# Kernel tuning notes

Measured on AMD Instinct MI355X. Metric: run time of the kernel, lower is better.

The kernel has to match this reference:

```python
import jax, jax.numpy as jnp
import numpy as np
from jax import lax

BG_THRESHOLD = -0.5
KEEP_COMPONENTS = 2
MIN_AREA = 200.0
N_ITERS = 32  # fixed label-propagation sweeps; each sweep does full-row/col run propagation + 3x3 max-pool (8-connectivity), plenty for blobby CT masks


def _conv_ones(x, k):
    kern = jnp.ones((1, 1, k, k), x.dtype)
    return lax.conv_general_dilated(x, kern, (1, 1), 'SAME',
                                    dimension_numbers=('NCHW', 'OIHW', 'NCHW'))


def _morph_open(m):
    # erode: all 9 neighbors set; dilate: any neighbor set (matches torch conv2d thresholds)
    e = (_conv_ones(m, 3) == 9.0).astype(m.dtype)
    return (_conv_ones(e, 3) > 0.0).astype(m.dtype)


def _fill_holes(m):
    # binary closing with 5x5 kernel
    d = (_conv_ones(m, 5) > 0.0).astype(m.dtype)
    return (_conv_ones(d, 5) == 25.0).astype(m.dtype)


def _prop_last(lab, msk):
    # propagate running max of labels along last axis, resetting at mask==0 (run propagation)
    lW = jnp.moveaxis(lab, -1, 0)  # [W,B,H]
    mW = jnp.moveaxis(msk, -1, 0)
    def step(c, lm):
        l, m = lm
        c = jnp.where(m, jnp.maximum(c, l), 0)
        return c, c
    _, out = lax.scan(step, jnp.zeros(lW.shape[1:], lab.dtype), (lW, mW))
    return jnp.moveaxis(out, 0, -1)


def _ccl_labels(msk):
    # 8-connected component labeling via iterative max-label propagation.
    # msk: bool [B,H,W]. Returns int32 labels (0 = background); pixels in the
    # same component converge to the same (max) seed label.
    B, H, W = msk.shape
    seeds = (jnp.arange(H * W, dtype=jnp.int32) + 1).reshape(H, W)
    lab0 = jnp.where(msk, seeds[None], 0)
    mi = msk.astype(jnp.int32)

    def body(i, lab):
        # diagonal hop (8-connectivity)
        lab = lax.reduce_window(lab, jnp.int32(0), lax.max,
                                (1, 3, 3), (1, 1, 1), 'SAME') * mi
        # full-run propagation left->right, right->left
        lab = _prop_last(lab, msk)
        lab = jnp.flip(_prop_last(jnp.flip(lab, -1), jnp.flip(msk, -1)), -1)
        # top->bottom, bottom->top
        labT = jnp.swapaxes(lab, -1, -2)
        mskT = jnp.swapaxes(msk, -1, -2)
        labT = _prop_last(labT, mskT)
        labT = jnp.flip(_prop_last(jnp.flip(labT, -1), jnp.flip(mskT, -1)), -1)
        return jnp.swapaxes(labT, -1, -2)

    return lax.fori_loop(0, N_ITERS, body, lab0)


def _keep_largest_components(mask4):
    # mask4: [B,1,H,W] float in {0,1}
    B, _, H, W = mask4.shape
    msk = mask4[:, 0] > 0.5
    labels = _ccl_labels(lax.stop_gradient(msk))  # int32 [B,H,W]
    # per-batch area histogram over label ids (label values in [0, H*W])
    def areas_fn(l, m):
        return jnp.zeros(H * W + 1, jnp.float32).at[l.ravel()].add(
            m.ravel().astype(jnp.float32))
    areas = jax.vmap(areas_fn)(labels, msk)          # [B, H*W+1]
    areas = areas.at[:, 0].set(0.0)                  # background excluded
    areas = jnp.where(areas >= MIN_AREA, areas, 0.0) # drop small noise regions
    topv, topi = lax.top_k(areas, KEEP_COMPONENTS)   # [B,K]
    topi = jnp.where(topv > 0.0, topi, -1)           # invalidate empty slots
    keep = jnp.any(labels[..., None] == topi[:, None, None, :], axis=-1)
    return keep.astype(mask4.dtype)[:, None]         # [B,1,H,W]


def setup_inputs() -> dict:
    key = jax.random.key(0)
    x = jax.random.normal(key, (64, 1, 512, 512), dtype=jnp.float32)
    return {"x": x}


def reference(x):
    m = (x > BG_THRESHOLD).astype(x.dtype)
    m = _morph_open(m)
    m = _keep_largest_components(m)
    m = _fill_holes(m)
    return m
```

## Files before the change

kernel.cpp:

```cpp
#include <hip/hip_runtime.h>
#include <stdint.h>
#include <limits.h>

#define BB 64
#define HH 512
#define WW 512
#define WPR 8
#define WPRP 9
#define HWP (HH*WW)
#define NPIX (BB*HWP)
#define NROWS (BB*HH)
#define RS 128
#define RSP 129
#define MAXRUNS (NROWS*RS)
#define KPR 32
#define MAXROOTS 2048

typedef unsigned char u8;
typedef unsigned long long u64;

__device__ __forceinline__ int imax(int a, int b){ return a > b ? a : b; }

__device__ __forceinline__ u64 hshift3_and(u64 c, u64 l, u64 r){
  return c & ((c << 1) | (l >> 63)) & ((c >> 1) | (r << 63));
}
__device__ __forceinline__ u64 hshift3_or(u64 c, u64 l, u64 r){
  return c | (c << 1) | (l >> 63) | (c >> 1) | (r << 63);
}
__device__ __forceinline__ u64 hshift5_and(u64 c, u64 l, u64 r){
  return hshift3_and(c, l, r) & ((c << 2) | (l >> 62)) & ((c >> 2) | (r << 62));
}
__device__ __forceinline__ u64 hshift5_or(u64 c, u64 l, u64 r){
  return hshift3_or(c, l, r) | (c << 2) | (l >> 62) | (c >> 2) | (r << 62);
}

__device__ __forceinline__ int lfind(int* lp, int p){
  while (true){
    int q = lp[p];
    int g = lp[q];
    if (q == g) return q;
    atomicMin(&lp[p], g);
    p = g;
  }
}
__device__ __forceinline__ void lunion(int* lp, int a, int b){
  while (true){
    a = lfind(lp, a);
    b = lfind(lp, b);
    if (a == b) return;
    if (a < b){ int t = a; a = b; b = t; }
    int old = atomicMin(&lp[a], b);
    if (old == a) return;
    a = old;
  }
}

#define ORPB 16
#define TPR (256/ORPB)
#define SLABN (ORPB*RS)
__global__ __launch_bounds__(256)
void k_thropen(const float* __restrict__ x, uint32_t* __restrict__ runs,
               int* __restrict__ cnt, int* __restrict__ parent,
               int* __restrict__ area, int* __restrict__ clabel,
               int* __restrict__ rootcnt){
  __shared__ u64 thr[ORPB + 4][WPRP];
  __shared__ u64 er[ORPB + 2][WPRP];
  __shared__ u64 dl[ORPB][WPRP];
  __shared__ uint32_t lruns[ORPB][RSP];
  __shared__ int lcnt[ORPB];
  __shared__ int lparent[SLABN];
  int R0 = blockIdx.x * ORPB;
  int img = R0 >> 9;
  int y0 = R0 & (HH - 1);
  int wid  = threadIdx.x >> 6;
  int lane = threadIdx.x & 63;
  if (blockIdx.x == 0 && threadIdx.x < BB) rootcnt[threadIdx.x] = 0;

  for (int pair = wid; pair < (ORPB + 4)/2; pair += 4){
    int lrow = 2*pair + (lane >> 5);
    int y = y0 - 2 + lrow;
    unsigned m = 0;
    if ((unsigned)y < (unsigned)HH){
      const float4* X = reinterpret_cast<const float4*>(
          x + ((size_t)img*HH + y)*WW + (lane & 31)*16);
      #pragma unroll
      for (int q = 0; q < 4; ++q){
        float4 vv = X[q];
        m |= (unsigned)(vv.x > -0.5f) << (q*4 + 0);
        m |= (unsigned)(vv.y > -0.5f) << (q*4 + 1);
        m |= (unsigned)(vv.z > -0.5f) << (q*4 + 2);
        m |= (unsigned)(vv.w > -0.5f) << (q*4 + 3);
      }
    }
    int sub = lane & 3;
    unsigned p1 = __shfl_xor(m, 1);
    unsigned v32 = (sub & 1) ? (p1 | (m << 16)) : (m | (p1 << 16));
    unsigned p2 = __shfl_xor(v32, 2);
    if (sub == 0)
      thr[lrow][(lane >> 2) & 7] = (u64)v32 | ((u64)p2 << 32);
  }
  __syncthreads();

  for (int s = threadIdx.x; s < (ORPB + 2)*WPR; s += 256){
    int j = s >> 3;
    int wi = s & 7;
    int rr = y0 - 1 + j;
    u64 acc = ~0ULL;
    #pragma unroll
    for (int dy = 0; dy < 3; ++dy){
      int ti = j + dy;
      u64 c = thr[ti][wi];
      u64 l = (wi > 0) ? thr[ti][wi-1] : 0ULL;
      u64 r = (wi < 7) ? thr[ti][wi+1] : 0ULL;
      acc &= hshift3_and(c, l, r);
    }
    if ((unsigned)rr >= (unsigned)HH) acc = 0ULL;
    er[j][wi] = acc;
  }
  __syncthreads();

  for (int s = threadIdx.x; s < ORPB*WPR; s += 256){
    int ri = s >> 3;
    int wi = s & 7;
    u64 acc = 0ULL;
    #pragma unroll
    for (int dy = 0; dy < 3; ++dy){
      int li = ri + dy;
      u64 c = er[li][wi];
      u64 l = (wi > 0) ? er[li][wi-1] : 0ULL;
      u64 r = (wi < 7) ? er[li][wi+1] : 0ULL;
      acc |= hshift3_or(c, l, r);
    }
    dl[ri][wi] = acc;
  }
  __syncthreads();

  for (int i = threadIdx.x; i < SLABN; i += 256) lparent[i] = i;

  if (threadIdx.x < ORPB){
    int ri = threadIdx.x;
    int r = R0 + ri;
    u64 w[8];
    #pragma unroll
    for (int i = 0; i < 8; ++i) w[i] = dl[ri][i];
    int base = r*RS;
    int k = 0;
    int pending = -1;
    u64 carry = 0;
    #pragma unroll
    for (int wi = 0; wi < 8; ++wi){
      u64 b = w[wi];
      u64 nb0 = (wi < 7) ? (w[wi+1] & 1ULL) : 0ULL;
      u64 starts = b & ~((b << 1) | carry);
      u64 ends   = b & ~(b >> 1);
      if (nb0) ends &= ~(1ULL << 63);
      carry = b >> 63;
      while (ends){
        int e = __ffsll((long long)ends) - 1; ends &= ends - 1;
        int s;
        if (pending >= 0){ s = pending; pending = -1; }
        else { s = wi*64 + (__ffsll((long long)starts) - 1); starts &= starts - 1; }
        uint32_t rv = (uint32_t)s | ((uint32_t)(wi*64 + e) << 16);
        int id = base + k;
        runs[id] = rv; lruns[ri][k] = rv;
        area[id] = 0; clabel[id] = 0;
        k++;
      }
      if (starts) pending = wi*64 + (__ffsll((long long)starts) - 1);
    }
    cnt[r] = k; lcnt[ri] = k;
  }
  __syncthreads();

  {
    int ri = threadIdx.x / TPR;
    int k0 = threadIdx.x % TPR;
    if (ri > 0){
      int ca = lcnt[ri], cb = lcnt[ri-1];
      if (cb > 0){
        for (int k = k0; k < ca; k += TPR){
          uint32_t ra = lruns[ri][k]; int sA = (int)(ra & 0xffff), eA = (int)(ra >> 16);
          int lo = 0, hi = cb, target = sA - 1;
          while (lo < hi){
            int mid = (lo + hi) >> 1;
            if ((int)(lruns[ri-1][mid] >> 16) < target) lo = mid + 1; else hi = mid;
          }
          for (int j = lo; j < cb; ++j){
            if ((int)(lruns[ri-1][j] & 0xffff) > eA + 1) break;
            lunion(lparent, ri*RS + k, (ri-1)*RS + j);
          }
        }
      }
    }
  }
  __syncthreads();

  {
    int ri = threadIdx.x / TPR;
    int k0 = threadIdx.x % TPR;
    int n = lcnt[ri];
    for (int k = k0; k < n; k += TPR){
      int lid = ri*RS + k;
      parent[R0*RS + lid] = R0*RS + lfind(lparent, lid);
    }
  }
}

__device__ __forceinline__ int uf_find(int* parent, int p){
  while (true){
    int q = parent[p];
    int g = parent[q];
    if (q == g) return q;
    atomicMin(&parent[p], g);
    p = g;
  }
}
__device__ __forceinline__ void uf_union(int* parent, int a, int b){
  while (true){
    a = uf_find(parent, a);
    b = uf_find(parent, b);
    if (a == b) return;
    if (a < b){ int t = a; a = b; b = t; }
    int old = atomicMin(&parent[a], b);
    if (old == a) return;
    a = old;
  }
}

__device__ __forceinline__ int ro_find(const int* __restrict__ parent, int p){
  while (true){ int q = parent[p]; if (q == p) return p; p = q; }
}

#define NBND (HH/ORPB - 1)
__global__ void k_linkb(const uint32_t* __restrict__ runs, const int* __restrict__ cnt,
                        int* __restrict__ parent){
  int t = blockIdx.x*blockDim.x + threadIdx.x;
  int bi = t >> 3, k0 = t & 7;
  if (bi >= BB*NBND) return;
  int img = bi / NBND, j = bi % NBND;
  int r = img*HH + (j + 1)*ORPB;
  int ca = cnt[r];
  int cb = cnt[r-1];
  if (cb == 0) return;
  const uint32_t* RB = runs + (size_t)(r-1)*RS;
  for (int k = k0; k < ca; k += 8){
    int id = r*RS + k;
    uint32_t ra = runs[id]; int sA = (int)(ra & 0xffff), eA = (int)(ra >> 16);
    int lo = 0, hi = cb, target = sA - 1;
    while (lo < hi){
      int mid = (lo + hi) >> 1;
      if ((int)(RB[mid] >> 16) < target) lo = mid + 1; else hi = mid;
    }
    for (int jj = lo; jj < cb; ++jj){
      uint32_t rb = RB[jj];
      if ((int)(rb & 0xffff) > eA + 1) break;
      uf_union(parent, id, (r-1)*RS + jj);
    }
  }
}

__global__ __launch_bounds__(256)
void k_slabacc(const uint32_t* __restrict__ runs, const int* __restrict__ cnt,
               int* __restrict__ parent, int* __restrict__ area,
               int* __restrict__ clabel){
  __shared__ int larea[SLABN];
  __shared__ int lclab[SLABN];
  for (int i = threadIdx.x; i < SLABN; i += 256){ larea[i] = 0; lclab[i] = 0; }
  __syncthreads();
  int R0 = blockIdx.x * ORPB;
  int base = R0 * RS;
  int y0 = R0 & (HH - 1);
  int ri = threadIdx.x / TPR;
  int k0 = threadIdx.x % TPR;
  int r = R0 + ri;
  int n = cnt[r];
  for (int k = k0; k < n; k += TPR){
    int id = r*RS + k;
    uint32_t run = runs[id]; int s = (int)(run & 0xffff), e = (int)(run >> 16);
    int len = e - s + 1;
    int labl = ri*WW + e + 1;
    int p = parent[id];
    int lid = p - base;
    if ((unsigned)lid < (unsigned)SLABN){
      atomicAdd(&larea[lid], len);
      atomicMax(&lclab[lid], labl);
    } else {
      p = ro_find(parent, p);
      atomicAdd(&area[p], len);
      atomicMax(&clabel[p], y0*WW + labl);
    }
  }
  __syncthreads();
  for (int i = threadIdx.x; i < SLABN; i += 256){
    int la = larea[i];
    if (la == 0) continue;
    int gid = base + i;
    int p = ro_find(parent, gid);
    atomicAdd(&area[p], la);
    atomicMax(&clabel[p], y0*WW + lclab[i]);
    if (p != gid) parent[gid] = p;
  }
}

__global__ void k_roots(const int* __restrict__ cnt, const int* __restrict__ parent,
                        const int* __restrict__ area, const int* __restrict__ clabel,
                        int* __restrict__ rootcnt, int* __restrict__ rootA,
                        int* __restrict__ rootL){
  int t = blockIdx.x*blockDim.x + threadIdx.x;
  if (t >= NROWS*KPR) return;
  int r = t / KPR, k0 = t % KPR;
  int n = cnt[r];
  int b = r >> 9;
  for (int k = k0; k < n; k += KPR){
    int id = r*RS + k;
    if (parent[id] != id) continue;
    int a = area[id];
    if (a < 200) continue;
    int idx = atomicAdd(&rootcnt[b], 1);
    rootA[b*MAXROOTS + idx] = a;
    rootL[b*MAXROOTS + idx] = clabel[id];
  }
}

__device__ __forceinline__ void ins2(int v, int i, int& v1, int& i1, int& v2, int& i2){
  if (v > v1 || (v == v1 && i < i1)) { v2 = v1; i2 = i1; v1 = v; i1 = i; }
  else if (v > v2 || (v == v2 && i < i2)) { v2 = v; i2 = i; }
}

__global__ void k_top2(const int* __restrict__ rootcnt, const int* __restrict__ rootA,
                       const int* __restrict__ rootL, int* __restrict__ keepL){
  __shared__ int sv1[64], si1[64], sv2[64], si2[64];
  int b = blockIdx.x;
  int n = rootcnt[b];
  int v1 = 0, i1 = INT_MAX, v2 = 0, i2 = INT_MAX;
  for (int k = threadIdx.x; k < n; k += 64)
    ins2(rootA[b*MAXROOTS + k], rootL[b*MAXROOTS + k], v1, i1, v2, i2);
  int t = threadIdx.x;
  sv1[t] = v1; si1[t] = i1; sv2[t] = v2; si2[t] = i2;
  __syncthreads();
  for (int s = 32; s > 0; s >>= 1){
    if (t < s){
      int a1 = sv1[t], b1 = si1[t], a2 = sv2[t], b2 = si2[t];
      ins2(sv1[t+s], si1[t+s], a1, b1, a2, b2);
      ins2(sv2[t+s], si2[t+s], a1, b1, a2, b2);
      sv1[t] = a1; si1[t] = b1; sv2[t] = a2; si2[t] = b2;
    }
    __syncthreads();
  }
  if (t == 0){
    keepL[b*2 + 0] = (sv1[0] > 0) ? si1[0] : 0;
    keepL[b*2 + 1] = (sv2[0] > 0) ? si2[0] : 0;
  }
}

__device__ __forceinline__ u64 rmask(int s, int e){
  u64 hi = (e >= 63) ? ~0ULL : ((1ULL << (e + 1)) - 1);
  u64 lo = (1ULL << s) - 1;
  return hi & ~lo;
}

#define CRPB 32
__global__ __launch_bounds__(256)
void k_closeexpand(const uint32_t* __restrict__ runs, const int* __restrict__ cnt,
                   const int* __restrict__ parent, const int* __restrict__ clabel,
                   const int* __restrict__ keepL, float* __restrict__ out){
  __shared__ u64 kp[CRPB + 8][WPR];
  __shared__ u64 dil[CRPB + 4][WPR];
  __shared__ u64 ero[CRPB][WPR];
  __shared__ int scnt[CRPB + 8];
  int R0 = blockIdx.x * CRPB;
  int img = R0 >> 9;
  int y0 = R0 & (HH - 1);
  int L1 = keepL[img*2], L2 = keepL[img*2 + 1];
  for (int i = threadIdx.x; i < (CRPB + 8)*WPR; i += 256)
    kp[i >> 3][i & 7] = 0ULL;
  if (threadIdx.x < CRPB + 8){
    int y = y0 + threadIdx.x - 4;
    scnt[threadIdx.x] = ((unsigned)y < (unsigned)HH) ? cnt[img*HH + y] : 0;
  }
  __syncthreads();
  for (int rr = threadIdx.x >> 3; rr < CRPB + 8; rr += 32){
    int y = y0 + rr - 4;
    int row = img*HH + y;
    int n = scnt[rr];
    for (int k = threadIdx.x & 7; k < n; k += 8){
      int id = row*RS + k;
      int p = parent[id];
      while (true){ int q = parent[p]; if (q == p) break; p = q; }
      int L = clabel[p];
      if (L != L1 && L != L2) continue;
      uint32_t run = runs[id]; int st = (int)(run & 0xffff), e = (int)(run >> 16);
      int w0 = st >> 6, w1 = e >> 6;
      if (w0 == w1) atomicOr(&kp[rr][w0], rmask(st & 63, e & 63));
      else {
        atomicOr(&kp[rr][w0], rmask(st & 63, 63));
        for (int wi = w0 + 1; wi < w1; ++wi) atomicOr(&kp[rr][wi], ~0ULL);
        atomicOr(&kp[rr][w1], rmask(0, e & 63));
      }
    }
  }
  __syncthreads();
  for (int s = threadIdx.x; s < (CRPB + 4)*WPR; s += 256){
    int li = s >> 3;
    int wi = s & 7;
    u64 acc = 0ULL;
    #pragma unroll
    for (int dy = -2; dy <= 2; ++dy){
      int ki = li + 2 + dy;
      u64 c = kp[ki][wi];
      u64 l = (wi > 0) ? kp[ki][wi-1] : 0ULL;
      u64 r = (wi < 7) ? kp[ki][wi+1] : 0ULL;
      acc |= hshift5_or(c, l, r);
    }
    dil[li][wi] = acc;
  }
  __syncthreads();
  for (int s = threadIdx.x; s < CRPB*WPR; s += 256){
    int ri = s >> 3;
    int wi = s & 7;
    int y = y0 + ri;
    u64 acc = ~0ULL;
    #pragma unroll
    for (int dy = -2; dy <= 2; ++dy){
      int yy = y + dy;
      u64 h;
      if ((unsigned)yy >= (unsigned)HH) h = 0ULL;
      else {
        int li = ri + 2 + dy;
        u64 c = dil[li][wi];
        u64 l = (wi > 0) ? dil[li][wi-1] : 0ULL;
        u64 r = (wi < 7) ? dil[li][wi+1] : 0ULL;
        h = hshift5_and(c, l, r);
      }
      acc &= h;
    }
    ero[ri][wi] = acc;
  }
  __syncthreads();
  float4* O = reinterpret_cast<float4*>(out + (size_t)R0*WW);
  for (int i = threadIdx.x; i < CRPB*WW/4; i += 256){
    int px = i * 4;
    int row = px >> 9;
    int x = px & (WW - 1);
    u64 word = ero[row][x >> 6];
    unsigned nib = (unsigned)((word >> (x & 63)) & 0xFULL);
    float4 f;
    f.x = (float)( nib       & 1);
    f.y = (float)((nib >> 1) & 1);
    f.z = (float)((nib >> 2) & 1);
    f.w = (float)((nib >> 3) & 1);
    O[i] = f;
  }
}

extern "C" void kernel_launch(void* const* d_in, const int* in_sizes, int n_in,
                              void* d_out, int out_size, void* d_ws, size_t ws_size,
                              hipStream_t stream){
  const float* x = (const float*)d_in[0];
  float* out = (float*)d_out;
  char* ws = (char*)d_ws;

  const size_t RUNS_OFF    = 0;
  const size_t PAR_OFF     = RUNS_OFF   + (size_t)MAXRUNS*4;
  const size_t AREA_OFF    = PAR_OFF    + (size_t)MAXRUNS*4;
  const size_t CLAB_OFF    = AREA_OFF   + (size_t)MAXRUNS*4;
  const size_t CNT_OFF     = CLAB_OFF   + (size_t)MAXRUNS*4;
  const size_t RCNT_OFF    = CNT_OFF    + (size_t)NROWS*4;
  const size_t RA_OFF      = RCNT_OFF   + 1024ull;
  const size_t RL_OFF      = RA_OFF     + (size_t)BB*MAXROOTS*4;
  const size_t KEEPL_OFF   = RL_OFF     + (size_t)BB*MAXROOTS*4;

  uint32_t* runs     = (uint32_t*)(ws + RUNS_OFF);
  int*      parent   = (int*)(ws + PAR_OFF);
  int*      area     = (int*)(ws + AREA_OFF);
  int*      clabel   = (int*)(ws + CLAB_OFF);
  int*      cnt      = (int*)(ws + CNT_OFF);
  int*      rootcnt  = (int*)(ws + RCNT_OFF);
  int*      rootA    = (int*)(ws + RA_OFF);
  int*      rootL    = (int*)(ws + RL_OFF);
  int*      keepL    = (int*)(ws + KEEPL_OFF);

  const int T = 256;
  dim3 blk(T);

  k_thropen<<<dim3(NROWS/ORPB), blk, 0, stream>>>(x, runs, cnt, parent, area,
                                                  clabel, rootcnt);
  k_linkb<<<dim3((BB*NBND*8 + T - 1)/T), blk, 0, stream>>>(runs, cnt, parent);
  k_slabacc<<<dim3(NROWS/ORPB), blk, 0, stream>>>(runs, cnt, parent, area, clabel);
  k_roots<<<dim3(NROWS*KPR/T), blk, 0, stream>>>(cnt, parent, area, clabel,
                                                 rootcnt, rootA, rootL);
  k_top2<<<dim3(BB), dim3(64), 0, stream>>>(rootcnt, rootA, rootL, keepL);
  k_closeexpand<<<dim3(NROWS/CRPB), blk, 0, stream>>>(runs, cnt, parent, clabel,
                                                      keepL, out);

  (void)in_sizes; (void)n_in; (void)out_size; (void)ws_size;
}
```

Before: 96.39 us.

## Split thresholding into a separate bit-packing kernel and halve close block rows

New measurement: 98.97 us. +2.7%, slower.

```diff
diff --git a/kernel.cpp b/kernel.cpp
--- a/kernel.cpp
+++ b/kernel.cpp
@@ -21,6 +21,30 @@
 
 __device__ __forceinline__ int imax(int a, int b){ return a > b ? a : b; }
 
+__global__ void k_threshpack(const float* __restrict__ x, u64* __restrict__ bits,
+                             int* __restrict__ rootcnt){
+  int t = blockIdx.x*blockDim.x + threadIdx.x;
+  if (t < BB) rootcnt[t] = 0;
+  const float4* X = reinterpret_cast<const float4*>(x) + (size_t)t*4;
+  unsigned m = 0;
+  #pragma unroll
+  for (int q = 0; q < 4; ++q){
+    float4 v = X[q];
+    m |= (unsigned)(v.x > -0.5f) << (q*4 + 0);
+    m |= (unsigned)(v.y > -0.5f) << (q*4 + 1);
+    m |= (unsigned)(v.z > -0.5f) << (q*4 + 2);
+    m |= (unsigned)(v.w > -0.5f) << (q*4 + 3);
+  }
+  int sub = t & 3;
+  unsigned p1 = __shfl_xor(m, 1);
+  unsigned v32 = (sub & 1) ? (p1 | (m << 16)) : (m | (p1 << 16));
+  unsigned p2 = __shfl_xor(v32, 2);
+  if ((sub & 3) == 0){
+    u64 w = (u64)v32 | ((u64)p2 << 32);
+    bits[t >> 2] = w;
+  }
+}
+
 __device__ __forceinline__ u64 hshift3_and(u64 c, u64 l, u64 r){
   return c & ((c << 1) | (l >> 63)) & ((c >> 1) | (r << 63));
 }
@@ -32,6 +56,12 @@
 }
 __device__ __forceinline__ u64 hshift5_or(u64 c, u64 l, u64 r){
   return hshift3_or(c, l, r) | (c << 2) | (l >> 62) | (c >> 2) | (r << 62);
+}
+
+__device__ __forceinline__ u64 ldw(const u64* __restrict__ in, int img, int rowInImg, int wi){
+  if ((unsigned)rowInImg >= (unsigned)HH) return 0ULL;
+  if ((unsigned)wi >= (unsigned)WPR) return 0ULL;
+  return in[((size_t)img*HH + rowInImg)*WPR + wi];
 }
 
 __device__ __forceinline__ int lfind(int* lp, int p){
@@ -59,11 +89,9 @@
 #define TPR (256/ORPB)
 #define SLABN (ORPB*RS)
 __global__ __launch_bounds__(256)
-void k_thropen(const float* __restrict__ x, uint32_t* __restrict__ runs,
-               int* __restrict__ cnt, int* __restrict__ parent,
-               int* __restrict__ area, int* __restrict__ clabel,
-               int* __restrict__ rootcnt){
-  __shared__ u64 thr[ORPB + 4][WPRP];
+void k_openlocal(const u64* __restrict__ bits, uint32_t* __restrict__ runs,
+                 int* __restrict__ cnt, int* __restrict__ parent,
+                 int* __restrict__ area, int* __restrict__ clabel){
   __shared__ u64 er[ORPB + 2][WPRP];
   __shared__ u64 dl[ORPB][WPRP];
   __shared__ uint32_t lruns[ORPB][RSP];
@@ -72,49 +100,21 @@
   int R0 = blockIdx.x * ORPB;
   int img = R0 >> 9;
   int y0 = R0 & (HH - 1);
-  int wid  = threadIdx.x >> 6;
-  int lane = threadIdx.x & 63;
-  if (blockIdx.x == 0 && threadIdx.x < BB) rootcnt[threadIdx.x] = 0;
-
-  for (int pair = wid; pair < (ORPB + 4)/2; pair += 4){
-    int lrow = 2*pair + (lane >> 5);
-    int y = y0 - 2 + lrow;
-    unsigned m = 0;
-    if ((unsigned)y < (unsigned)HH){
-      const float4* X = reinterpret_cast<const float4*>(
-          x + ((size_t)img*HH + y)*WW + (lane & 31)*16);
-      #pragma unroll
-      for (int q = 0; q < 4; ++q){
-        float4 vv = X[q];
-        m |= (unsigned)(vv.x > -0.5f) << (q*4 + 0);
-        m |= (unsigned)(vv.y > -0.5f) << (q*4 + 1);
-        m |= (unsigned)(vv.z > -0.5f) << (q*4 + 2);
-        m |= (unsigned)(vv.w > -0.5f) << (q*4 + 3);
-      }
-    }
-    int sub = lane & 3;
-    unsigned p1 = __shfl_xor(m, 1);
-    unsigned v32 = (sub & 1) ? (p1 | (m << 16)) : (m | (p1 << 16));
-    unsigned p2 = __shfl_xor(v32, 2);
-    if (sub == 0)
-      thr[lrow][(lane >> 2) & 7] = (u64)v32 | ((u64)p2 << 32);
-  }
-  __syncthreads();
 
   for (int s = threadIdx.x; s < (ORPB + 2)*WPR; s += 256){
     int j = s >> 3;
     int wi = s & 7;
-    int rr = y0 - 1 + j;
+    int yy = y0 - 1 + j;
     u64 acc = ~0ULL;
     #pragma unroll
-    for (int dy = 0; dy < 3; ++dy){
-      int ti = j + dy;
-      u64 c = thr[ti][wi];
-      u64 l = (wi > 0) ? thr[ti][wi-1] : 0ULL;
-      u64 r = (wi < 7) ? thr[ti][wi+1] : 0ULL;
-      acc &= hshift3_and(c, l, r);
-    }
-    if ((unsigned)rr >= (unsigned)HH) acc = 0ULL;
+    for (int dy = -1; dy <= 1; ++dy){
+      int y = yy + dy;
+      u64 c = ldw(bits, img, y, wi);
+      u64 l = ldw(bits, img, y, wi - 1);
+      u64 r = ldw(bits, img, y, wi + 1);
+      acc &= ((unsigned)y < (unsigned)HH) ? hshift3_and(c, l, r) : 0ULL;
+    }
+    if ((unsigned)yy >= (unsigned)HH) acc = 0ULL;
     er[j][wi] = acc;
   }
   __syncthreads();
@@ -359,7 +359,7 @@
   return hi & ~lo;
 }
 
-#define CRPB 32
+#define CRPB 16
 __global__ __launch_bounds__(256)
 void k_closeexpand(const uint32_t* __restrict__ runs, const int* __restrict__ cnt,
                    const int* __restrict__ parent, const int* __restrict__ clabel,
@@ -460,7 +460,8 @@
   float* out = (float*)d_out;
   char* ws = (char*)d_ws;
 
-  const size_t RUNS_OFF    = 0;
+  const size_t BITS_OFF    = 0;
+  const size_t RUNS_OFF    = BITS_OFF   + 2097152ull;
   const size_t PAR_OFF     = RUNS_OFF   + (size_t)MAXRUNS*4;
   const size_t AREA_OFF    = PAR_OFF    + (size_t)MAXRUNS*4;
   const size_t CLAB_OFF    = AREA_OFF   + (size_t)MAXRUNS*4;
@@ -470,6 +471,7 @@
   const size_t RL_OFF      = RA_OFF     + (size_t)BB*MAXROOTS*4;
   const size_t KEEPL_OFF   = RL_OFF     + (size_t)BB*MAXROOTS*4;
 
+  u64*      bits     = (u64*)(ws + BITS_OFF);
   uint32_t* runs     = (uint32_t*)(ws + RUNS_OFF);
   int*      parent   = (int*)(ws + PAR_OFF);
   int*      area     = (int*)(ws + AREA_OFF);
@@ -483,8 +485,9 @@
   const int T = 256;
   dim3 blk(T);
 
-  k_thropen<<<dim3(NROWS/ORPB), blk, 0, stream>>>(x, runs, cnt, parent, area,
-                                                  clabel, rootcnt);
+  k_threshpack<<<dim3(NPIX/16/T), blk, 0, stream>>>(x, bits, rootcnt);
+  k_openlocal<<<dim3(NROWS/ORPB), blk, 0, stream>>>(bits, runs, cnt, parent,
+                                                    area, clabel);
   k_linkb<<<dim3((BB*NBND*8 + T - 1)/T), blk, 0, stream>>>(runs, cnt, parent);
   k_slabacc<<<dim3(NROWS/ORPB), blk, 0, stream>>>(runs, cnt, parent, area, clabel);
   k_roots<<<dim3(NROWS*KPR/T), blk, 0, stream>>>(cnt, parent, area, clabel,
```
